# Kernel tuning notes

Measured on AMD Instinct MI355X. Metric: run time of the kernel, lower is better.

The kernel has to match this reference:

```python
import jax, jax.numpy as jnp
import numpy as np
from jax import lax

CIN, COUT, K, PAD = 256, 128, 3, 1


def setup_inputs() -> dict:
    key = jax.random.key(0)
    ks = jax.random.split(key, 5)
    N, h0, w0 = 2, 64, 64
    x = jax.random.normal(ks[0], (N, CIN, h0, w0), jnp.float32)
    lateral_feat = jax.random.normal(ks[1], (N, COUT, 1, 1), jnp.float32)
    trans_w = jax.random.normal(ks[2], (CIN, COUT, K, K), jnp.float32) * 0.02
    off_w1 = jax.random.normal(ks[3], (64, COUT, 3, 3), jnp.float32) * 0.02
    off_b1 = jnp.zeros((64,), jnp.float32)
    off_w2 = jax.random.normal(ks[4], (2 * K * K, 64, 3, 3), jnp.float32) * 0.02
    off_b2 = jnp.zeros((2 * K * K,), jnp.float32)
    return dict(x=x, lateral_feat=lateral_feat, trans_w=trans_w,
                off_w1=off_w1, off_b1=off_b1, off_w2=off_w2, off_b2=off_b2)


def _conv2d(x, w, b, pad):
    y = lax.conv_general_dilated(x, w, (1, 1), [(pad, pad), (pad, pad)],
                                 dimension_numbers=('NCHW', 'OIHW', 'NCHW'))
    return y + b[None, :, None, None]


def _conv_transpose2d(x, w, stride, pad, out_pad):
    # torch ConvTranspose2d weight layout: [Cin, Cout, k, k]
    k = w.shape[2]
    wt = jnp.flip(w, (2, 3)).transpose(1, 0, 2, 3)  # [Cout, Cin, k, k]
    lo = k - 1 - pad
    hi = k - 1 - pad + out_pad
    return lax.conv_general_dilated(x, wt, (1, 1), [(lo, hi), (lo, hi)],
                                    lhs_dilation=(stride, stride),
                                    dimension_numbers=('NCHW', 'OIHW', 'NCHW'))


def _deform_conv2d(x, offset, w, pad):
    # x [N,C,H,W], offset [N,2*K*K,H,W] (y,x interleaved per kernel tap), w [O,C,K,K]
    N, C, H, W = x.shape
    O = w.shape[0]
    KK = K * K
    off = offset.reshape(N, KK, 2, H, W)
    ky = jnp.arange(KK) // K
    kx = jnp.arange(KK) % K
    py = jnp.arange(H)[None, None, :, None] + (ky - pad)[None, :, None, None] + off[:, :, 0]
    px = jnp.arange(W)[None, None, None, :] + (kx - pad)[None, :, None, None] + off[:, :, 1]
    y0 = jnp.floor(py)
    x0 = jnp.floor(px)
    dy = py - y0
    dx = px - x0
    y0i = y0.astype(jnp.int32)
    x0i = x0.astype(jnp.int32)
    xf = x.reshape(N, C, H * W)

    def corner(yi, xi, wgt):
        valid = (yi >= 0) & (yi < H) & (xi >= 0) & (xi < W)
        idx = (jnp.clip(yi, 0, H - 1) * W + jnp.clip(xi, 0, W - 1)).reshape(N, -1)
        v = jnp.take_along_axis(xf, idx[:, None, :], axis=2).reshape(N, C, KK, H, W)
        return v * (wgt * valid)[:, None]

    sampled = (corner(y0i, x0i, (1 - dy) * (1 - dx))
               + corner(y0i, x0i + 1, (1 - dy) * dx)
               + corner(y0i + 1, x0i, dy * (1 - dx))
               + corner(y0i + 1, x0i + 1, dy * dx))  # [N,C,KK,H,W]
    return jnp.einsum('nckhw,ock->nohw', sampled, w.reshape(O, C, KK))


def reference(x, lateral_feat, trans_w, off_w1, off_b1, off_w2, off_b2):
    up = _conv_transpose2d(x, trans_w, 2, PAD, 1)          # [N, COUT, 2h0, 2w0]
    h = jax.nn.relu(_conv2d(lateral_feat, off_w1, off_b1, 1))
    offset = jnp.tanh(_conv2d(h, off_w2, off_b2, 1))       # [N, 18, 1, 1]
    N, C, H, W = up.shape
    # offset.repeat(1, 1, H, W) with 1x1 spatial input == broadcast to full grid
    offset = jnp.broadcast_to(offset, (N, 2 * K * K, H, W))
    # deform_conv2d uses trans_conv weight [O=CIN, I=COUT, K, K], stride=1, pad=PAD
    return _deform_conv2d(up, offset, trans_w, PAD)        # [N, CIN, H, W]
```

## Files before the change

kernel.cpp:

```cpp
#include <hip/hip_runtime.h>
#include <hip/hip_fp16.h>
#include <math.h>

typedef __attribute__((ext_vector_type(8))) _Float16 f16x8;
typedef __attribute__((ext_vector_type(4))) float f32x4;

__device__ __forceinline__ unsigned short f2h(float f) {
    __half h = __float2half_rn(f);
    union { __half h; unsigned short u; } v; v.h = h; return v.u;
}
__device__ __forceinline__ unsigned pk2h(float lo, float hi) {
    __half2 h = __floats2half2_rn(lo, hi);
    union { __half2 h; unsigned u; } v; v.h = h; return v.u;
}

#define BARRIER() do { asm volatile("s_waitcnt lgkmcnt(0)" ::: "memory"); \
                       __builtin_amdgcn_s_barrier(); } while (0)

__device__ __forceinline__ void blend_store_h(uint4 uA, uint4 uB, uint4 uC, uint4 uD,
                                              __half2 w0, __half2 w1, __half2 w2, __half2 w3,
                                              unsigned short* dst) {
    union U { uint4 u; __half2 h[4]; };
    U a, b, c, d, r;
    a.u = uA; b.u = uB; c.u = uC; d.u = uD;
#pragma unroll
    for (int i = 0; i < 4; ++i)
        r.h[i] = __hfma2(w0, a.h[i], __hfma2(w1, b.h[i], __hfma2(w2, c.h[i], __hmul2(w3, d.h[i]))));
    *(uint4*)dst = r.u;
}

__global__ __launch_bounds__(256) void k_prep(const float* __restrict__ x,
                                              const float* __restrict__ lat,
                                              const float* __restrict__ tw,
                                              const float* __restrict__ w1,
                                              const float* __restrict__ b1,
                                              const float* __restrict__ w2,
                                              const float* __restrict__ b2,
                                              unsigned short* __restrict__ xp,
                                              unsigned short* __restrict__ A2f,
                                              unsigned short* __restrict__ Awf,
                                              unsigned short* __restrict__ upp,
                                              int* __restrict__ ipar,
                                              float* __restrict__ fpar) {
    __shared__ float sm[8420];
    int b = blockIdx.x, t = threadIdx.x;
    if (b == 0) {
        for (int i = t; i < 8192; i += 256) sm[(i >> 7) * 129 + (i & 127)] = w1[i * 9 + 4];
        __syncthreads();
        if (t < 128) {
            int n = t >> 6, o = t & 63;
            float s = b1[o];
            const float* ln = lat + n * 128;
#pragma unroll 8
            for (int c = 0; c < 128; ++c) s += ln[c] * sm[o * 129 + c];
            sm[8256 + t] = fmaxf(s, 0.f);
        }
        __syncthreads();
        if (t < 36) {
            int n = t / 18, j = t % 18;
            float s = b2[j];
            for (int o = 0; o < 64; ++o) s += sm[8256 + n * 64 + o] * w2[(j * 64 + o) * 9 + 4];
            float ov = tanhf(s);
            ov = fminf(fmaxf(ov, -0.999999f), 0.999999f);
            sm[8384 + t] = ov;
        }
        __syncthreads();
        if (t < 36) {
            int n = t / 18, j = t % 18;
            int tap = j >> 1, d = j & 1;
            float ov = sm[8384 + t];
            float fl = floorf(ov);
            int kc = d ? (tap % 3) : (tap / 3);
            ipar[(n * 9 + tap) * 2 + d] = kc - 1 + (int)fl;
            fpar[(n * 9 + tap) * 2 + d] = ov - fl;
        }
    } else if (b < 145) {
        int slot = (b - 1) * 256 + t;
        int l = slot & 63;
        int mi = (slot >> 6) & 3;
        int w = (slot >> 8) & 3;
        int k = slot >> 10;
        int row = w * 64 + mi * 16 + (l & 15);
        int kq = l >> 4;
        unsigned short v[8];
#pragma unroll
        for (int j = 0; j < 8; ++j) {
            int kcol = k * 32 + kq * 8 + j;
            int tap = kcol >> 7, c = kcol & 127;
            v[j] = f2h(tw[(row * 128 + c) * 9 + tap]);
        }
        unsigned p0 = (unsigned)v[0] | ((unsigned)v[1] << 16);
        unsigned p1 = (unsigned)v[2] | ((unsigned)v[3] << 16);
        unsigned p2 = (unsigned)v[4] | ((unsigned)v[5] << 16);
        unsigned p3 = (unsigned)v[6] | ((unsigned)v[7] << 16);
        *(uint4*)(A2f + slot * 8) = make_uint4(p0, p1, p2, p3);
    } else if (b < 289) {
        int slot = (b - 145) * 256 + t;
        int l = slot & 63;
        int mi = (slot >> 6) & 3;
        int wm = (slot >> 8) & 1;
        int k = slot >> 9;
        int row = wm * 64 + mi * 16 + (l & 15);
        int kq = l >> 4;
        unsigned short v[8];
#pragma unroll
        for (int j = 0; j < 8; ++j) {
            int kcol = k * 32 + kq * 8 + j;
            int t9 = kcol >> 8, ci = kcol & 255;
            int ky = t9 / 3, kx = t9 - ky * 3;
            v[j] = f2h(tw[(ci * 128 + row) * 9 + (2 - ky) * 3 + (2 - kx)]);
        }
        unsigned p0 = (unsigned)v[0] | ((unsigned)v[1] << 16);
        unsigned p1 = (unsigned)v[2] | ((unsigned)v[3] << 16);
        unsigned p2 = (unsigned)v[4] | ((unsigned)v[5] << 16);
        unsigned p3 = (unsigned)v[6] | ((unsigned)v[7] << 16);
        *(uint4*)(Awf + slot * 8) = make_uint4(p0, p1, p2, p3);
    } else if (b < 801) {
        int bb = b - 289;
        int h = bb & 63, cq = (bb >> 6) & 3, n = bb >> 8;
        int c0 = cq * 64;
        {
            int wcol = t & 63, sub = t >> 6;
            for (int r = 0; r < 16; ++r) {
                int ci_l = r * 4 + sub;
                sm[ci_l * 65 + wcol] = x[((n * 256 + c0 + ci_l) * 64 + h) * 64 + wcol];
            }
        }
        __syncthreads();
        int wcol = t >> 2, cg = t & 3;
        unsigned short* dst = xp + (size_t)n * (65 * 65 * 256) + (h * 65 + wcol) * 256 + c0 + cg * 16;
        unsigned pk[8];
#pragma unroll
        for (int j = 0; j < 8; ++j)
            pk[j] = pk2h(sm[(cg * 16 + 2 * j) * 65 + wcol], sm[(cg * 16 + 2 * j + 1) * 65 + wcol]);
        *(uint4*)dst = make_uint4(pk[0], pk[1], pk[2], pk[3]);
        *(uint4*)(dst + 8) = make_uint4(pk[4], pk[5], pk[6], pk[7]);
    } else {
        int g = (b - 801) * 256 + t;
        int n2 = g >= 16640 ? 1 : 0;
        int i = g - n2 * 16640;
        int px_id = i >> 4, chv = i & 15;
        int r, c;
        if (px_id < 528) {
            int rr = px_id / 132;
            r = rr < 2 ? rr : 128 + rr;
            c = px_id - rr * 132;
        } else {
            int jj = px_id - 528;
            r = 2 + (jj >> 2);
            int cc = jj & 3;
            c = cc < 2 ? cc : 128 + cc;
        }
        uint4* p = (uint4*)(upp + (size_t)n2 * (132 * 132 * 128) + ((r * 132 + c) * 128) + chv * 8);
        *p = make_uint4(0u, 0u, 0u, 0u);
    }
}

__global__ __launch_bounds__(256) void k_tconv3(const unsigned short* __restrict__ xp,
                                                const unsigned short* __restrict__ Awf,
                                                unsigned short* __restrict__ upp) {
    __shared__ unsigned short Bs[2][2][64][40];
    __shared__ int st9[4];
    __shared__ int sbb[4];
    int t = threadIdx.x;
    int b = blockIdx.x;
    int phase = b & 1;
    int xpar = ((b >> 1) & 1) ^ phase;
    int n = (b >> 2) & 1;
    int yh = b >> 3;
    int y = yh * 2 + phase;
    const unsigned short* xpn = xp + (size_t)n * (65 * 65 * 256);

    int lane = t & 63, w = t >> 6;
    int col = lane & 15, q = lane >> 4;
    int wm = w >> 1, wn = w & 1;
    int bx = t >> 2, bcg = t & 3;
    int boff = bx * 256 + bcg * 8;

    int kys[2], kxs[2], nky, nkx;
    if (phase) { kys[0] = 0; kys[1] = 2; nky = 2; } else { kys[0] = 1; kys[1] = 1; nky = 1; }
    if (xpar)  { kxs[0] = 0; kxs[1] = 2; nkx = 2; } else { kxs[0] = 1; kxs[1] = 1; nkx = 1; }
    int nslots = nky * nkx;
    if (t < 4) {
        int tc = t < nslots ? t : 0;
        int a1 = (nkx == 2) ? (tc >> 1) : tc;
        int a2 = (nkx == 2) ? (tc & 1) : 0;
        int ky = kys[a1], kx = kxs[a2];
        st9[t] = ky * 3 + kx;
        int d2 = (y + ky - 1) >> 1;
        int s = (xpar + kx - 1) >> 1;
        sbb[t] = (d2 * 65 + s) * 256;
    }
    int NPAIR = nslots * 4;

    f32x4 acc[4][2];
#pragma unroll
    for (int mi = 0; mi < 4; ++mi)
#pragma unroll
        for (int ni = 0; ni < 2; ++ni) acc[mi][ni] = (f32x4){0.f, 0.f, 0.f, 0.f};

    __syncthreads();

    const unsigned short* Afw = Awf + wm * 2048 + lane * 8;
    f16x8 aC[2][4], aN[2][4];
    uint4 nb0, nb1;

    {
        const unsigned short* pT = xpn + sbb[0] + boff;
        uint4 b0 = *(const uint4*)pT;
        uint4 b1 = *(const uint4*)(pT + 32);
        const unsigned short* ap = Afw + st9[0] * 32768;
#pragma unroll
        for (int mi = 0; mi < 4; ++mi) {
            aC[0][mi] = *(const f16x8*)(ap + mi * 512);
            aC[1][mi] = *(const f16x8*)(ap + 4096 + mi * 512);
        }
        *(uint4*)&Bs[0][0][bx][bcg * 8] = b0;
        *(uint4*)&Bs[0][1][bx][bcg * 8] = b1;
    }
    BARRIER();

#define TC_PH(PP, BUF, AC, AN)                                                   \
    {                                                                            \
        int P_ = (PP);                                                           \
        if (P_ + 1 < NPAIR) {                                                    \
            int slot_ = (P_ + 1) >> 2;                                           \
            int cb0_ = ((P_ + 1) & 3) * 2;                                       \
            const unsigned short* pT_ = xpn + sbb[slot_] + cb0_ * 32 + boff;     \
            nb0 = *(const uint4*)pT_;                                            \
            nb1 = *(const uint4*)(pT_ + 32);                                     \
            const unsigned short* ap_ = Afw + (st9[slot_] * 8 + cb0_) * 4096;    \
            _Pragma("unroll")                                                    \
            for (int mi = 0; mi < 4; ++mi) {                                     \
                AN[0][mi] = *(const f16x8*)(ap_ + mi * 512);                     \
                AN[1][mi] = *(const f16x8*)(ap_ + 4096 + mi * 512);              \
            }                                                                    \
        }                                                                        \
        f16x8 bb[2][2];                                                          \
        _Pragma("unroll")                                                        \
        for (int c = 0; c < 2; ++c)                                              \
            _Pragma("unroll")                                                    \
            for (int ni = 0; ni < 2; ++ni)                                       \
                bb[c][ni] = *(const f16x8*)&Bs[BUF][c][wn * 32 + ni * 16 + col][q * 8]; \
        _Pragma("unroll")                                                        \
        for (int c = 0; c < 2; ++c)                                              \
            _Pragma("unroll")                                                    \
            for (int mi = 0; mi < 4; ++mi)                                       \
                _Pragma("unroll")                                                \
                for (int ni = 0; ni < 2; ++ni)                                   \
                    acc[mi][ni] = __builtin_amdgcn_mfma_f32_16x16x32_f16(AC[c][mi], bb[c][ni], acc[mi][ni], 0, 0, 0); \
        if (P_ + 1 < NPAIR) {                                                    \
            *(uint4*)&Bs[BUF ^ 1][0][bx][bcg * 8] = nb0;                         \
            *(uint4*)&Bs[BUF ^ 1][1][bx][bcg * 8] = nb1;                         \
        }                                                                        \
        BARRIER();                                                               \
    }

    for (int pp = 0; pp < NPAIR; pp += 2) {
        TC_PH(pp,     0, aC, aN);
        TC_PH(pp + 1, 1, aN, aC);
    }
#undef TC_PH

    unsigned short* uppn = upp + (size_t)n * (132 * 132 * 128);
#pragma unroll
    for (int mi = 0; mi < 4; ++mi)
#pragma unroll
        for (int ni = 0; ni < 2; ++ni) {
            int co = wm * 64 + mi * 16 + q * 4;
            int p64 = wn * 32 + ni * 16 + col;
            int xg = 2 * p64 + xpar;
            unsigned short* p = uppn + ((y + 2) * 132 + (xg + 2)) * 128 + co;
            unsigned lo = pk2h(acc[mi][ni][0], acc[mi][ni][1]);
            unsigned hi = pk2h(acc[mi][ni][2], acc[mi][ni][3]);
            *(uint2*)p = make_uint2(lo, hi);
        }
}

__global__ __launch_bounds__(256) void k_deform4(const unsigned short* __restrict__ upp,
                                                 const unsigned short* __restrict__ A2f,
                                                 const int* __restrict__ ipar,
                                                 const float* __restrict__ fpar,
                                                 float* __restrict__ out) {
    __shared__ unsigned short Ws[2][5][68][32];
    __shared__ unsigned short Bs[2][2][64][40];
    __shared__ int sR0[9], sDx[9];
    __shared__ __half2 swh[9][4];
    int t = threadIdx.x;
    int b = blockIdx.x;
    int xcd = b & 7, j = b >> 3;
    int n = xcd >> 2, band = xcd & 3;
    int y = band * 32 + (j & 31);
    int tx0 = (j >> 5) * 64;
    const unsigned short* uppn = upp + (size_t)n * (132 * 132 * 128);

    int lane = t & 63, w = t >> 6;
    int col = lane & 15, q = lane >> 4;
    int bx = t >> 2, bcg = t & 3;

    if (t < 9) {
        int iy = ipar[(n * 9 + t) * 2 + 0], ix = ipar[(n * 9 + t) * 2 + 1];
        float fy = fpar[(n * 9 + t) * 2 + 0], fx = fpar[(n * 9 + t) * 2 + 1];
        sR0[t] = iy + 2;
        sDx[t] = ix + 2;
        swh[t][0] = __float2half2_rn((1.f - fy) * (1.f - fx));
        swh[t][1] = __float2half2_rn((1.f - fy) * fx);
        swh[t][2] = __float2half2_rn(fy * (1.f - fx));
        swh[t][3] = __float2half2_rn(fy * fx);
    }

    f32x4 acc[4][4];
#pragma unroll
    for (int mi = 0; mi < 4; ++mi)
#pragma unroll
        for (int ni = 0; ni < 4; ++ni) acc[mi][ni] = (f32x4){0.f, 0.f, 0.f, 0.f};

    __syncthreads();

    const unsigned short* Afw = A2f + w * 2048 + lane * 8;
    f16x8 aC[2][4], aN[2][4];

#define BLEND_WS(CHUNK, TAP, DST)                                                \
    {                                                                            \
        int r0_ = sR0[TAP], dx_ = sDx[TAP];                                      \
        const unsigned short* pA_ = &Ws[CHUNK][0][0][0] + (r0_ * 68 + bx + dx_) * 32 + bcg * 8; \
        uint4 uA_ = *(const uint4*)pA_;                                          \
        uint4 uB_ = *(const uint4*)(pA_ + 32);                                   \
        uint4 uC_ = *(const uint4*)(pA_ + 68 * 32);                              \
        uint4 uD_ = *(const uint4*)(pA_ + 68 * 32 + 32);                         \
        blend_store_h(uA_, uB_, uC_, uD_, swh[TAP][0], swh[TAP][1],              \
                      swh[TAP][2], swh[TAP][3], DST);                            \
    }

#define DEF_TAU(TAU, BUF, AC, AN, S)                                             \
    {                                                                            \
        if ((TAU) < 8) {                                                         \
            const unsigned short* ap_ = Afw + (((TAU) + 1) * 4 + (S) * 2) * 8192;\
            _Pragma("unroll")                                                    \
            for (int mi = 0; mi < 4; ++mi) {                                     \
                AN[0][mi] = *(const f16x8*)(ap_ + mi * 512);                     \
                AN[1][mi] = *(const f16x8*)(ap_ + 8192 + mi * 512);              \
            }                                                                    \
        }                                                                        \
        f16x8 bb[2][4];                                                          \
        _Pragma("unroll")                                                        \
        for (int c = 0; c < 2; ++c)                                              \
            _Pragma("unroll")                                                    \
            for (int ni = 0; ni < 4; ++ni)                                       \
                bb[c][ni] = *(const f16x8*)&Bs[BUF][c][ni * 16 + col][q * 8];    \
        _Pragma("unroll")                                                        \
        for (int c = 0; c < 2; ++c)                                              \
            _Pragma("unroll")                                                    \
            for (int mi = 0; mi < 4; ++mi)                                       \
                _Pragma("unroll")                                                \
                for (int ni = 0; ni < 4; ++ni)                                   \
                    acc[mi][ni] = __builtin_amdgcn_mfma_f32_16x16x32_f16(AC[c][mi], bb[c][ni], acc[mi][ni], 0, 0, 0); \
        if ((TAU) < 8) {                                                         \
            BLEND_WS(0, (TAU) + 1, &Bs[BUF ^ 1][0][bx][bcg * 8]);                \
            BLEND_WS(1, (TAU) + 1, &Bs[BUF ^ 1][1][bx][bcg * 8]);                \
        }                                                                        \
        BARRIER();                                                               \
    }

    for (int s = 0; s < 2; ++s) {
        for (int i = t; i < 2720; i += 256) {
            int c2 = i / 1360;
            int rem2 = i - c2 * 1360;
            int row = rem2 / 272;
            int rem = rem2 - row * 272;
            int px = rem >> 2, cg4 = rem & 3;
            uint4 v = *(const uint4*)&uppn[(size_t)((y + row) * 132 + tx0 + px) * 128 + s * 64 + c2 * 32 + cg4 * 8];
            *(uint4*)(&Ws[c2][0][0][0] + (row * 68 + px) * 32 + cg4 * 8) = v;
        }
        BARRIER();
        {
            const unsigned short* ap0 = Afw + s * 16384;
#pragma unroll
            for (int mi = 0; mi < 4; ++mi) {
                aC[0][mi] = *(const f16x8*)(ap0 + mi * 512);
                aC[1][mi] = *(const f16x8*)(ap0 + 8192 + mi * 512);
            }
            BLEND_WS(0, 0, &Bs[0][0][bx][bcg * 8]);
            BLEND_WS(1, 0, &Bs[0][1][bx][bcg * 8]);
        }
        BARRIER();
        DEF_TAU(0, 0, aC, aN, s);
        DEF_TAU(1, 1, aN, aC, s);
        DEF_TAU(2, 0, aC, aN, s);
        DEF_TAU(3, 1, aN, aC, s);
        DEF_TAU(4, 0, aC, aN, s);
        DEF_TAU(5, 1, aN, aC, s);
        DEF_TAU(6, 0, aC, aN, s);
        DEF_TAU(7, 1, aN, aC, s);
        DEF_TAU(8, 0, aC, aN, s);
    }
#undef DEF_TAU
#undef BLEND_WS

#pragma unroll
    for (int mi = 0; mi < 4; ++mi)
#pragma unroll
        for (int ni = 0; ni < 4; ++ni) {
            int o = w * 64 + mi * 16 + q * 4;
            int xg = tx0 + ni * 16 + col;
            float* p = out + (((size_t)(n * 256 + o)) * 128 + y) * 128 + xg;
            p[0]         = acc[mi][ni][0];
            p[16384]     = acc[mi][ni][1];
            p[2 * 16384] = acc[mi][ni][2];
            p[3 * 16384] = acc[mi][ni][3];
        }
}

extern "C" void kernel_launch(void* const* d_in, const int* in_sizes, int n_in,
                              void* d_out, int out_size, void* d_ws, size_t ws_size,
                              hipStream_t stream) {
    const float* x   = (const float*)d_in[0];
    const float* lat = (const float*)d_in[1];
    const float* tw  = (const float*)d_in[2];
    const float* w1  = (const float*)d_in[3];
    const float* b1  = (const float*)d_in[4];
    const float* w2  = (const float*)d_in[5];
    const float* b2  = (const float*)d_in[6];
    float* out = (float*)d_out;

    char* ws = (char*)d_ws;
    unsigned short* upp = (unsigned short*)ws;
    unsigned short* xp  = (unsigned short*)(ws + 8921088);
    unsigned short* A2f = (unsigned short*)(ws + 13247488);
    unsigned short* Awf = (unsigned short*)(ws + 13837312);
    int*   ipar         = (int*)(ws + 14427136);
    float* fpar         = (float*)(ws + 14427424);

    hipMemsetAsync(ws + 8921088, 0, 4326400, stream);
    k_prep<<<931, 256, 0, stream>>>(x, lat, tw, w1, b1, w2, b2, xp, A2f, Awf, upp, ipar, fpar);
    k_tconv3<<<512, 256, 0, stream>>>(xp, Awf, upp);
    k_deform4<<<512, 256, 0, stream>>>(upp, A2f, ipar, fpar, out);
}
```

Measured before the change: 131.2 us.

## Stage weight repacking through LDS and double the K-chunk per tconv pipeline stage

The prep kernel's weight-repacking blocks now read a contiguous slab of trans_w with float4 loads, convert it to fp16 in shared memory, and gather the MFMA fragment layout from LDS. The old code did strided scalar global reads. The transposed-conv kernel now processes four 32-channel chunks per pipeline stage instead of two. This halves the number of barriers and iterations but doubles the register footprint for A fragments and the LDS B buffers. More registers could lower occupancy.

Measured after the change: 133.3 us. Within noise of the previous version (+1.6%).

```diff
diff --git a/kernel.cpp b/kernel.cpp
--- a/kernel.cpp
+++ b/kernel.cpp
@@ -42,7 +42,9 @@
                                               unsigned short* __restrict__ upp,
                                               int* __restrict__ ipar,
                                               float* __restrict__ fpar) {
-    __shared__ float sm[8420];
+    __shared__ char smraw[36864];
+    float* sm = (float*)smraw;
+    unsigned short* smh = (unsigned short*)smraw;
     int b = blockIdx.x, t = threadIdx.x;
     if (b == 0) {
         for (int i = t; i < 8192; i += 256) sm[(i >> 7) * 129 + (i & 127)] = w1[i * 9 + 4];
@@ -75,41 +77,62 @@
             fpar[(n * 9 + tap) * 2 + d] = ov - fl;
         }
     } else if (b < 145) {
-        int slot = (b - 1) * 256 + t;
-        int l = slot & 63;
-        int mi = (slot >> 6) & 3;
-        int w = (slot >> 8) & 3;
-        int k = slot >> 10;
-        int row = w * 64 + mi * 16 + (l & 15);
+        int bb_ = b - 1;
+        int k = bb_ >> 2, w = bb_ & 3;
+        int tap = k >> 2;
+        int c0 = (k & 3) * 32;
+        for (int i = t * 4; i < 18432; i += 1024) {
+            int r = i / 288;
+            int cc = i - r * 288;
+            const float* src = tw + (size_t)((w * 64 + r) * 128 + c0) * 9 + cc;
+            float4 v4 = *(const float4*)src;
+            smh[r * 288 + cc + 0] = f2h(v4.x);
+            smh[r * 288 + cc + 1] = f2h(v4.y);
+            smh[r * 288 + cc + 2] = f2h(v4.z);
+            smh[r * 288 + cc + 3] = f2h(v4.w);
+        }
+        __syncthreads();
+        int slot = bb_ * 256 + t;
+        int l = t & 63;
+        int mi = (t >> 6) & 3;
+        int row_l = mi * 16 + (l & 15);
         int kq = l >> 4;
         unsigned short v[8];
 #pragma unroll
-        for (int j = 0; j < 8; ++j) {
-            int kcol = k * 32 + kq * 8 + j;
-            int tap = kcol >> 7, c = kcol & 127;
-            v[j] = f2h(tw[(row * 128 + c) * 9 + tap]);
-        }
+        for (int j = 0; j < 8; ++j)
+            v[j] = smh[row_l * 288 + (kq * 8 + j) * 9 + tap];
         unsigned p0 = (unsigned)v[0] | ((unsigned)v[1] << 16);
         unsigned p1 = (unsigned)v[2] | ((unsigned)v[3] << 16);
         unsigned p2 = (unsigned)v[4] | ((unsigned)v[5] << 16);
         unsigned p3 = (unsigned)v[6] | ((unsigned)v[7] << 16);
         *(uint4*)(A2f + slot * 8) = make_uint4(p0, p1, p2, p3);
     } else if (b < 289) {
-        int slot = (b - 145) * 256 + t;
-        int l = slot & 63;
-        int mi = (slot >> 6) & 3;
-        int wm = (slot >> 8) & 1;
-        int k = slot >> 9;
-        int row = wm * 64 + mi * 16 + (l & 15);
+        int bb_ = b - 145;
+        int k = bb_ >> 1, wm = bb_ & 1;
+        int t9 = k >> 3;
+        int ci0 = (k & 7) * 32;
+        int ky = t9 / 3, kx = t9 - ky * 3;
+        int tapf = (2 - ky) * 3 + (2 - kx);
+        for (int i = t * 4; i < 18432; i += 1024) {
+            int cil = i / 576;
+            int rr = i - cil * 576;
+            const float* src = tw + (size_t)((ci0 + cil) * 128 + wm * 64) * 9 + rr;
+            float4 v4 = *(const float4*)src;
+            smh[cil * 576 + rr + 0] = f2h(v4.x);
+            smh[cil * 576 + rr + 1] = f2h(v4.y);
+            smh[cil * 576 + rr + 2] = f2h(v4.z);
+            smh[cil * 576 + rr + 3] = f2h(v4.w);
+        }
+        __syncthreads();
+        int slot = bb_ * 256 + t;
+        int l = t & 63;
+        int mi = (t >> 6) & 3;
+        int row_l = mi * 16 + (l & 15);
         int kq = l >> 4;
         unsigned short v[8];
 #pragma unroll
-        for (int j = 0; j < 8; ++j) {
-            int kcol = k * 32 + kq * 8 + j;
-            int t9 = kcol >> 8, ci = kcol & 255;
-            int ky = t9 / 3, kx = t9 - ky * 3;
-            v[j] = f2h(tw[(ci * 128 + row) * 9 + (2 - ky) * 3 + (2 - kx)]);
-        }
+        for (int j = 0; j < 8; ++j)
+            v[j] = smh[(kq * 8 + j) * 576 + row_l * 9 + tapf];
         unsigned p0 = (unsigned)v[0] | ((unsigned)v[1] << 16);
         unsigned p1 = (unsigned)v[2] | ((unsigned)v[3] << 16);
         unsigned p2 = (unsigned)v[4] | ((unsigned)v[5] << 16);
@@ -156,10 +179,10 @@
     }
 }
 
-__global__ __launch_bounds__(256) void k_tconv3(const unsigned short* __restrict__ xp,
+__global__ __launch_bounds__(256) void k_tconv4(const unsigned short* __restrict__ xp,
                                                 const unsigned short* __restrict__ Awf,
                                                 unsigned short* __restrict__ upp) {
-    __shared__ unsigned short Bs[2][2][64][40];
+    __shared__ unsigned short Bs[2][4][64][40];
     __shared__ int st9[4];
     __shared__ int sbb[4];
     int t = threadIdx.x;
@@ -191,7 +214,7 @@
         int s = (xpar + kx - 1) >> 1;
         sbb[t] = (d2 * 65 + s) * 256;
     }
-    int NPAIR = nslots * 4;
+    int NQ = nslots * 2;
 
     f32x4 acc[4][2];
 #pragma unroll
@@ -202,63 +225,71 @@
     __syncthreads();
 
     const unsigned short* Afw = Awf + wm * 2048 + lane * 8;
-    f16x8 aC[2][4], aN[2][4];
-    uint4 nb0, nb1;
+    f16x8 aC[4][4], aN[4][4];
+    uint4 nb0, nb1, nb2, nb3;
 
     {
         const unsigned short* pT = xpn + sbb[0] + boff;
         uint4 b0 = *(const uint4*)pT;
         uint4 b1 = *(const uint4*)(pT + 32);
+        uint4 b2 = *(const uint4*)(pT + 64);
+        uint4 b3 = *(const uint4*)(pT + 96);
         const unsigned short* ap = Afw + st9[0] * 32768;
 #pragma unroll
-        for (int mi = 0; mi < 4; ++mi) {
-            aC[0][mi] = *(const f16x8*)(ap + mi * 512);
-            aC[1][mi] = *(const f16x8*)(ap + 4096 + mi * 512);
-        }
+        for (int c = 0; c < 4; ++c)
+#pragma unroll
+            for (int mi = 0; mi < 4; ++mi)
+                aC[c][mi] = *(const f16x8*)(ap + c * 4096 + mi * 512);
         *(uint4*)&Bs[0][0][bx][bcg * 8] = b0;
         *(uint4*)&Bs[0][1][bx][bcg * 8] = b1;
+        *(uint4*)&Bs[0][2][bx][bcg * 8] = b2;
+        *(uint4*)&Bs[0][3][bx][bcg * 8] = b3;
     }
     BARRIER();
 
-#define TC_PH(PP, BUF, AC, AN)                                                   \
+#define TC_PH(QQ, BUF, AC, AN)                                                   \
     {                                                                            \
-        int P_ = (PP);                                                           \
-        if (P_ + 1 < NPAIR) {                                                    \
-            int slot_ = (P_ + 1) >> 2;                                           \
-            int cb0_ = ((P_ + 1) & 3) * 2;                                       \
+        int Q_ = (QQ);                                                           \
+        if (Q_ + 1 < NQ) {                                                       \
+            int slot_ = (Q_ + 1) >> 1;                                           \
+            int cb0_ = ((Q_ + 1) & 1) * 4;                                       \
             const unsigned short* pT_ = xpn + sbb[slot_] + cb0_ * 32 + boff;     \
             nb0 = *(const uint4*)pT_;                                            \
             nb1 = *(const uint4*)(pT_ + 32);                                     \
+            nb2 = *(const uint4*)(pT_ + 64);                                     \
+            nb3 = *(const uint4*)(pT_ + 96);                                     \
             const unsigned short* ap_ = Afw + (st9[slot_] * 8 + cb0_) * 4096;    \
             _Pragma("unroll")                                                    \
-            for (int mi = 0; mi < 4; ++mi) {                                     \
-                AN[0][mi] = *(const f16x8*)(ap_ + mi * 512);                     \
-                AN[1][mi] = *(const f16x8*)(ap_ + 4096 + mi * 512);              \
-            }                                                                    \
+            for (int c = 0; c < 4; ++c)                                          \
+                _Pragma("unroll")                                                \
+                for (int mi = 0; mi < 4; ++mi)                                   \
+                    AN[c][mi] = *(const f16x8*)(ap_ + c * 4096 + mi * 512);      \
         }                                                                        \
-        f16x8 bb[2][2];                                                          \
+        f16x8 bb[4][2];                                                          \
         _Pragma("unroll")                                                        \
-        for (int c = 0; c < 2; ++c)                                              \
+        for (int c = 0; c < 4; ++c)                                              \
             _Pragma("unroll")                                                    \
             for (int ni = 0; ni < 2; ++ni)                                       \
                 bb[c][ni] = *(const f16x8*)&Bs[BUF][c][wn * 32 + ni * 16 + col][q * 8]; \
         _Pragma("unroll")                                                        \
-        for (int c = 0; c < 2; ++c)                                              \
+        for (int c = 0; c < 4; ++c)                                              \
             _Pragma("unroll")                                                    \
             for (int mi = 0; mi < 4; ++mi)                                       \
                 _Pragma("unroll")                                                \
                 for (int ni = 0; ni < 2; ++ni)                                   \
                     acc[mi][ni] = __builtin_amdgcn_mfma_f32_16x16x32_f16(AC[c][mi], bb[c][ni], acc[mi][ni], 0, 0, 0); \
-        if (P_ + 1 < NPAIR) {                                                    \
+        if (Q_ + 1 < NQ) {                                                       \
             *(uint4*)&Bs[BUF ^ 1][0][bx][bcg * 8] = nb0;                         \
             *(uint4*)&Bs[BUF ^ 1][1][bx][bcg * 8] = nb1;                         \
+            *(uint4*)&Bs[BUF ^ 1][2][bx][bcg * 8] = nb2;                         \
+            *(uint4*)&Bs[BUF ^ 1][3][bx][bcg * 8] = nb3;                         \
         }                                                                        \
         BARRIER();                                                               \
     }
 
-    for (int pp = 0; pp < NPAIR; pp += 2) {
-        TC_PH(pp,     0, aC, aN);
-        TC_PH(pp + 1, 1, aN, aC);
+    for (int qq = 0; qq < NQ; qq += 2) {
+        TC_PH(qq,     0, aC, aN);
+        TC_PH(qq + 1, 1, aN, aC);
     }
 #undef TC_PH
 
@@ -433,6 +464,6 @@
 
     hipMemsetAsync(ws + 8921088, 0, 4326400, stream);
     k_prep<<<931, 256, 0, stream>>>(x, lat, tw, w1, b1, w2, b2, xp, A2f, Awf, upp, ipar, fpar);
-    k_tconv3<<<512, 256, 0, stream>>>(xp, Awf, upp);
+    k_tconv4<<<512, 256, 0, stream>>>(xp, Awf, upp);
     k_deform4<<<512, 256, 0, stream>>>(upp, A2f, ipar, fpar, out);
 }
```
